# Kernel tuning notes

Hardware: AMD Instinct MI355X
Metric: run time of the kernel (lower is better)

The kernel has to match this reference:

```python
import jax, jax.numpy as jnp
import numpy as np
import math

B, S, D, H = 8, 1024, 1024, 16
HD = D // H  # head_features = 64
SCALE = math.sqrt(HD)


def setup_inputs() -> dict:
    key = jax.random.key(0)
    k0, k1, k2, k3, k4 = jax.random.split(key, 5)
    x = jax.random.normal(k0, (B, S, D), dtype=jnp.float32)
    attn_mask = (jax.random.uniform(k1, (B, S, S)) < 0.9).astype(jnp.float32)
    w_scale = 1.0 / math.sqrt(D)  # keep unsafe exp in finite range
    Wq = jax.random.normal(k2, (D, D), dtype=jnp.float32) * w_scale
    Wk = jax.random.normal(k3, (D, D), dtype=jnp.float32) * w_scale
    Wv = jax.random.normal(k4, (D, D), dtype=jnp.float32) * w_scale
    return {"x": x, "attn_mask": attn_mask, "Wq": Wq, "Wk": Wk, "Wv": Wv}


def reference(x, attn_mask, Wq, Wk, Wv):
    b, s, _ = x.shape

    def split_heads(t):  # [b,s,D] -> [b,H,s,HD]
        return t.reshape(b, s, H, HD).transpose(0, 2, 1, 3)

    q = split_heads(x @ Wq)
    k = split_heads(x @ Wk)
    v = split_heads(x @ Wv)

    # unsafe softmax: exp without max subtraction, multiplicative mask, +1e-8 denom
    scores = jnp.einsum('bhsd,bhtd->bhst', q, k) / SCALE
    e = jnp.exp(scores) * attn_mask[:, None, :, :]
    w = e / (e.sum(axis=3, keepdims=True) + 1e-8)

    ctx = jnp.einsum('bhst,bhtd->bhsd', w, v)  # [b,H,s,HD]
    return ctx.transpose(0, 2, 1, 3).reshape(b, s, D)
```

## Files before the change

### kernel.cpp

```cpp
#include <hip/hip_runtime.h>

#define KDIM 1024

typedef _Float16 half8 __attribute__((ext_vector_type(8)));
typedef _Float16 half4 __attribute__((ext_vector_type(4)));
typedef __fp16 fp16x2 __attribute__((ext_vector_type(2)));
typedef __fp16 fp16x4 __attribute__((ext_vector_type(4)));
typedef float f32x4 __attribute__((ext_vector_type(4)));

#if defined(__has_builtin)
#if __has_builtin(__builtin_amdgcn_global_load_lds)
#define HAVE_GLDS 1
#endif
#if __has_builtin(__builtin_amdgcn_exp2f)
#define EXP2(x) __builtin_amdgcn_exp2f(x)
#endif
#if __has_builtin(__builtin_amdgcn_cvt_pkrtz)
#define HAVE_PKRTZ 1
#endif
#if __has_builtin(__builtin_amdgcn_fdot2)
#define HAVE_FDOT2 1
#endif
#endif
#ifndef EXP2
#define EXP2(x) exp2f(x)
#endif

__device__ __forceinline__ void stage16(const _Float16* g, _Float16* wave_base, int lane) {
#ifdef HAVE_GLDS
  __builtin_amdgcn_global_load_lds(
      (const __attribute__((address_space(1))) void*)g,
      (__attribute__((address_space(3))) void*)wave_base, 16, 0, 0);
#else
  *(half8*)(wave_base + lane * 8) = *(const half8*)g;
#endif
}

__global__ void cast_x_kernel(const float* __restrict__ x, _Float16* __restrict__ xb) {
  size_t i = ((size_t)blockIdx.x * 256 + threadIdx.x) * 4;
  float4 v = *(const float4*)(x + i);
  half4 h = { (_Float16)v.x, (_Float16)v.y, (_Float16)v.z, (_Float16)v.w };
  *(half4*)(xb + i) = h;
}

__global__ void wtrans_kernel(const float* __restrict__ Wq, const float* __restrict__ Wk,
                              const float* __restrict__ Wv, _Float16* __restrict__ Wqkvt) {
  int z = blockIdx.z;
  const float* src = z == 0 ? Wq : (z == 1 ? Wk : Wv);
  _Float16* dst = Wqkvt + (size_t)z * KDIM * KDIM;
  float sc = (z == 0) ? 0.18033688011112042f : 1.0f;
  __shared__ _Float16 tile[32][33];
  int tx = threadIdx.x & 31, ty = threadIdx.x >> 5;
  int c0 = blockIdx.x * 32, r0 = blockIdx.y * 32;
#pragma unroll
  for (int i = 0; i < 4; i++) {
    int r = r0 + ty + i * 8;
    tile[tx][ty + i * 8] = (_Float16)(src[(size_t)r * KDIM + c0 + tx] * sc);
  }
  __syncthreads();
#pragma unroll
  for (int i = 0; i < 4; i++) {
    int n = c0 + ty + i * 8;
    dst[(size_t)n * KDIM + r0 + tx] = tile[ty + i * 8][tx];
  }
}

__global__ void maskbits_kernel(const float* __restrict__ m, unsigned long long* __restrict__ bits) {
  size_t i = (size_t)blockIdx.x * 256 + threadIdx.x;
  unsigned long long b = __ballot(m[i] != 0.0f);
  if ((threadIdx.x & 63) == 0) bits[i >> 6] = b;
}

__global__ __launch_bounds__(256, 2)
void gemm_kernel(const _Float16* __restrict__ A, const _Float16* __restrict__ Bt,
                 _Float16* __restrict__ Qt, _Float16* __restrict__ Kh,
                 _Float16* __restrict__ Vth) {
  __shared__ _Float16 As[128 * 32];
  __shared__ _Float16 Bs[128 * 32];
  int tid = threadIdx.x;
  int lane = tid & 63, w4 = tid >> 6;
  int la = lane & 15, qd = lane >> 4;
  int wm = w4 & 1, wn = w4 >> 1;
  int m0 = blockIdx.y * 128, n0 = blockIdx.x * 128;
  int r = tid >> 2, c = (tid & 3) * 8;
  const _Float16* Ag = A + (size_t)(m0 + r) * KDIM + c;
  const _Float16* Bg = Bt + (size_t)(n0 + r) * KDIM + c;
  _Float16* a0 = As + w4 * 512;
  _Float16* b0 = Bs + w4 * 512;
  f32x4 acc[4][4] = {};
  for (int kt = 0; kt < KDIM; kt += 32) {
    stage16(Ag + kt, a0, lane);
    stage16(Ag + (size_t)64 * KDIM + kt, a0 + 2048, lane);
    stage16(Bg + kt, b0, lane);
    stage16(Bg + (size_t)64 * KDIM + kt, b0 + 2048, lane);
    __syncthreads();
    half8 af[4], bf[4];
#pragma unroll
    for (int mi = 0; mi < 4; mi++)
      af[mi] = *(const half8*)(As + (wm * 64 + mi * 16 + la) * 32 + qd * 8);
#pragma unroll
    for (int ni = 0; ni < 4; ni++)
      bf[ni] = *(const half8*)(Bs + (wn * 64 + ni * 16 + la) * 32 + qd * 8);
#pragma unroll
    for (int mi = 0; mi < 4; mi++)
#pragma unroll
      for (int ni = 0; ni < 4; ni++)
        acc[mi][ni] = __builtin_amdgcn_mfma_f32_16x16x32_f16(af[mi], bf[ni], acc[mi][ni], 0, 0, 0);
    __syncthreads();
  }
  int which = n0 >> 10;
  int hh = ((n0 + wn * 64) >> 6) & 15;
  int mbase = m0 + wm * 64;
  int b = mbase >> 10, s0 = mbase & 1023;
  if (which == 1) {
#pragma unroll
    for (int mi = 0; mi < 4; mi++)
#pragma unroll
      for (int ni = 0; ni < 4; ni++) {
        f32x4 v = acc[mi][ni];
        int s = s0 + mi * 16 + qd * 4;
        int d = ni * 16 + la;
#pragma unroll
        for (int rg = 0; rg < 4; rg++)
          Kh[(((size_t)(b * 16 + hh)) * 1024 + s + rg) * 64 + d] = (_Float16)v[rg];
      }
  } else {
    _Float16* dst = (which == 0) ? Qt : Vth;
    _Float16* ep = (w4 < 2) ? (As + w4 * 2048) : (Bs + (w4 - 2) * 2048);
    _Float16* base = dst + ((size_t)(b * 16 + hh)) * 64 * 1024;
    int rr = lane >> 2, c4 = lane & 3;
#pragma unroll
    for (int ni = 0; ni < 4; ni++) {
#pragma unroll
      for (int mi = 0; mi < 4; mi++) {
        f32x4 v = acc[mi][ni];
        half4 hv = { (_Float16)v[0], (_Float16)v[1], (_Float16)v[2], (_Float16)v[3] };
        *(half4*)(ep + la * 72 + mi * 16 + qd * 4) = hv;
      }
      half8 o0 = *(const half8*)(ep + rr * 72 + c4 * 16);
      half8 o1 = *(const half8*)(ep + rr * 72 + c4 * 16 + 8);
      _Float16* gp = base + (size_t)(ni * 16 + rr) * 1024 + s0 + c4 * 16;
      *(half8*)gp = o0;
      *(half8*)(gp + 8) = o1;
    }
  }
}

__global__ __launch_bounds__(512, 2)
void attn_kernel(const _Float16* __restrict__ Qt, const _Float16* __restrict__ K,
                 const _Float16* __restrict__ Vt, const unsigned long long* __restrict__ mbits,
                 float* __restrict__ out) {
  __shared__ _Float16 Ks[2 * 64 * 32];
  __shared__ _Float16 Vs[2 * 64 * 40];
  int tid = threadIdx.x;
  int lane = tid & 63, w4 = tid >> 6;
  int la = lane & 15, qd = lane >> 4;
  int linear = blockIdx.x;
  int xlo = linear & 7;
  int tmp = linear >> 3;
  int qt = tmp & 7;
  int hb = (tmp >> 3) * 8 + xlo;
  int h = hb & 15, b = hb >> 4;
  const _Float16* Qp = Qt + ((size_t)(b * 16 + h)) * 64 * 1024;
  const _Float16* Kp = K + ((size_t)(b * 16 + h)) * 1024 * 64;
  const _Float16* Vp = Vt + ((size_t)(b * 16 + h)) * 64 * 1024;
  int q0w = qt * 128 + w4 * 16;
  half8 qf[2];
#pragma unroll
  for (int ks = 0; ks < 2; ks++)
#pragma unroll
    for (int j = 0; j < 8; j++)
      qf[ks][j] = Qp[(size_t)(ks * 32 + qd * 8 + j) * 1024 + q0w + la];
  unsigned long long mq[4];
  {
    const ulonglong2* mp =
        (const ulonglong2*)(mbits + ((size_t)b * 1024 + q0w + la) * 16 + qd * 4);
    ulonglong2 m01 = mp[0];
    ulonglong2 m23 = mp[1];
    mq[0] = m01.x; mq[1] = m01.y; mq[2] = m23.x; mq[3] = m23.y;
  }
  f32x4 acco[4] = {};
  float rs = 0.0f;
  int kt_t = (tid & 255) >> 2;
  int kt_d = (tid >> 8) * 32 + (tid & 3) * 8;
  _Float16* kbase = Ks + w4 * 512;
  int vd = tid >> 3;
  int vt = (tid & 7) * 8;
  _Float16* vdst = Vs + (vt >= 32 ? 2560 : 0) + vd * 40 + (vt & 31);
#ifdef HAVE_FDOT2
  fp16x2 one2 = { (__fp16)1.0f, (__fp16)1.0f };
#endif
  for (int tt = 0; tt < 16; tt++) {
    half8 vv = *(const half8*)(Vp + (size_t)vd * 1024 + tt * 64 + vt);
    stage16(Kp + (size_t)(tt * 64 + kt_t) * 64 + kt_d, kbase, lane);
    *(half8*)vdst = vv;
    __syncthreads();
    f32x4 accs[4] = {};
#pragma unroll
    for (int tsub = 0; tsub < 4; tsub++)
#pragma unroll
      for (int ks = 0; ks < 2; ks++) {
        half8 kf = *(const half8*)(Ks + ks * 2048 + (tsub * 16 + la) * 32 + qd * 8);
        accs[tsub] = __builtin_amdgcn_mfma_f32_16x16x32_f16(kf, qf[ks], accs[tsub], 0, 0, 0);
      }
    unsigned long long mw = __shfl(mq[tt & 3], ((tt >> 2) << 4) + la);
#pragma unroll
    for (int tsub = 0; tsub < 4; tsub++) {
      float e0 = ((mw >> (tsub * 16 + qd * 4 + 0)) & 1ull) ? EXP2(accs[tsub][0]) : 0.0f;
      float e1 = ((mw >> (tsub * 16 + qd * 4 + 1)) & 1ull) ? EXP2(accs[tsub][1]) : 0.0f;
      float e2 = ((mw >> (tsub * 16 + qd * 4 + 2)) & 1ull) ? EXP2(accs[tsub][2]) : 0.0f;
      float e3 = ((mw >> (tsub * 16 + qd * 4 + 3)) & 1ull) ? EXP2(accs[tsub][3]) : 0.0f;
      half4 pf;
#ifdef HAVE_PKRTZ
      fp16x2 p01 = __builtin_amdgcn_cvt_pkrtz(e0, e1);
      fp16x2 p23 = __builtin_amdgcn_cvt_pkrtz(e2, e3);
      fp16x4 pfv = __builtin_shufflevector(p01, p23, 0, 1, 2, 3);
      pf = __builtin_bit_cast(half4, pfv);
#else
      pf[0] = (_Float16)e0; pf[1] = (_Float16)e1; pf[2] = (_Float16)e2; pf[3] = (_Float16)e3;
#endif
#if defined(HAVE_FDOT2) && defined(HAVE_PKRTZ)
      rs = __builtin_amdgcn_fdot2(p01, one2, rs, false);
      rs = __builtin_amdgcn_fdot2(p23, one2, rs, false);
#else
      rs += e0 + e1 + e2 + e3;
#endif
#pragma unroll
      for (int nsub = 0; nsub < 4; nsub++) {
        half4 vf = *(const half4*)(Vs + (tsub >> 1) * 2560 + (nsub * 16 + la) * 40 +
                                   (tsub & 1) * 16 + qd * 4);
        acco[nsub] = __builtin_amdgcn_mfma_f32_16x16x16f16(pf, vf, acco[nsub], 0, 0, 0);
      }
    }
    __syncthreads();
  }
  rs += __shfl_xor(rs, 16);
  rs += __shfl_xor(rs, 32);
  float inv_q = 1.0f / (rs + 1e-8f);
  float* op = out + (size_t)b * 1024 * 1024 + (size_t)h * 64;
#pragma unroll
  for (int rg = 0; rg < 4; rg++) {
    float inv = __shfl(inv_q, qd * 4 + rg);
    int s = q0w + qd * 4 + rg;
#pragma unroll
    for (int nsub = 0; nsub < 4; nsub++)
      op[(size_t)s * 1024 + nsub * 16 + la] = acco[nsub][rg] * inv;
  }
}

extern "C" void kernel_launch(void* const* d_in, const int* in_sizes, int n_in,
                              void* d_out, int out_size, void* d_ws, size_t ws_size,
                              hipStream_t stream) {
  (void)in_sizes; (void)n_in; (void)out_size; (void)ws_size;
  const float* x = (const float*)d_in[0];
  const float* am = (const float*)d_in[1];
  const float* Wq = (const float*)d_in[2];
  const float* Wk = (const float*)d_in[3];
  const float* Wv = (const float*)d_in[4];
  float* out = (float*)d_out;

  char* p = (char*)d_ws;
  _Float16* xb = (_Float16*)p;    p += (size_t)8192 * 1024 * 2;
  _Float16* Wqkvt = (_Float16*)p; p += (size_t)3 * 1024 * 1024 * 2;
  _Float16* Qt = (_Float16*)p;    p += (size_t)8192 * 1024 * 2;
  _Float16* Kh = (_Float16*)p;    p += (size_t)8192 * 1024 * 2;
  _Float16* Vth = (_Float16*)p;   p += (size_t)8192 * 1024 * 2;
  unsigned long long* mb = (unsigned long long*)p;

  cast_x_kernel<<<8192, 256, 0, stream>>>(x, xb);
  wtrans_kernel<<<dim3(32, 32, 3), 256, 0, stream>>>(Wq, Wk, Wv, Wqkvt);
  maskbits_kernel<<<32768, 256, 0, stream>>>(am, mb);
  gemm_kernel<<<dim3(24, 64), 256, 0, stream>>>(xb, Wqkvt, Qt, Kh, Vth);
  attn_kernel<<<1024, 512, 0, stream>>>(Qt, Kh, Vth, mb, out);
}
```

Measured before the change: 266.2 us.

## Process two query tiles per wave to reuse staged K/V tiles

Each attention block now covers 256 query rows instead of 128, with every wave holding two 16-row query fragments. Each K/V tile loaded into shared memory serves twice as many queries, and each K fragment read from LDS feeds two MFMAs. This halves the K/V global traffic and staging per query. In exchange the grid shrinks to 512 blocks, which may reduce occupancy and load balance, and register pressure rises under launch_bounds(512,2).

```diff
diff --git a/kernel.cpp b/kernel.cpp
--- a/kernel.cpp
+++ b/kernel.cpp
@@ -158,36 +158,39 @@
   int linear = blockIdx.x;
   int xlo = linear & 7;
   int tmp = linear >> 3;
-  int qt = tmp & 7;
-  int hb = (tmp >> 3) * 8 + xlo;
+  int qt = tmp & 3;
+  int hb = (tmp >> 2) * 8 + xlo;
   int h = hb & 15, b = hb >> 4;
-  const _Float16* Qp = Qt + ((size_t)(b * 16 + h)) * 64 * 1024;
-  const _Float16* Kp = K + ((size_t)(b * 16 + h)) * 1024 * 64;
-  const _Float16* Vp = Vt + ((size_t)(b * 16 + h)) * 64 * 1024;
-  int q0w = qt * 128 + w4 * 16;
-  half8 qf[2];
-#pragma unroll
-  for (int ks = 0; ks < 2; ks++)
-#pragma unroll
-    for (int j = 0; j < 8; j++)
-      qf[ks][j] = Qp[(size_t)(ks * 32 + qd * 8 + j) * 1024 + q0w + la];
-  unsigned long long mq[4];
-  {
+  const _Float16* Qp = Qt + (size_t)hb * 64 * 1024;
+  const _Float16* Kp = K + (size_t)hb * 1024 * 64;
+  const _Float16* Vp = Vt + (size_t)hb * 64 * 1024;
+  int q0w = qt * 256 + w4 * 16;
+  half8 qf[2][2];
+#pragma unroll
+  for (int qi = 0; qi < 2; qi++)
+#pragma unroll
+    for (int ks = 0; ks < 2; ks++)
+#pragma unroll
+      for (int j = 0; j < 8; j++)
+        qf[qi][ks][j] = Qp[(size_t)(ks * 32 + qd * 8 + j) * 1024 + q0w + qi * 128 + la];
+  unsigned long long mq[2][4];
+#pragma unroll
+  for (int qi = 0; qi < 2; qi++) {
     const ulonglong2* mp =
-        (const ulonglong2*)(mbits + ((size_t)b * 1024 + q0w + la) * 16 + qd * 4);
+        (const ulonglong2*)(mbits + ((size_t)b * 1024 + q0w + qi * 128 + la) * 16 + qd * 4);
     ulonglong2 m01 = mp[0];
     ulonglong2 m23 = mp[1];
-    mq[0] = m01.x; mq[1] = m01.y; mq[2] = m23.x; mq[3] = m23.y;
-  }
-  f32x4 acco[4] = {};
-  float rs = 0.0f;
+    mq[qi][0] = m01.x; mq[qi][1] = m01.y; mq[qi][2] = m23.x; mq[qi][3] = m23.y;
+  }
+  f32x4 acco[2][4] = {};
+  float rs[2] = {0.f, 0.f};
   int kt_t = (tid & 255) >> 2;
   int kt_d = (tid >> 8) * 32 + (tid & 3) * 8;
   _Float16* kbase = Ks + w4 * 512;
   int vd = tid >> 3;
   int vt = (tid & 7) * 8;
   _Float16* vdst = Vs + (vt >= 32 ? 2560 : 0) + vd * 40 + (vt & 31);
-#ifdef HAVE_FDOT2
+#if defined(HAVE_FDOT2) && defined(HAVE_PKRTZ)
   fp16x2 one2 = { (__fp16)1.0f, (__fp16)1.0f };
 #endif
   for (int tt = 0; tt < 16; tt++) {
@@ -195,56 +198,67 @@
     stage16(Kp + (size_t)(tt * 64 + kt_t) * 64 + kt_d, kbase, lane);
     *(half8*)vdst = vv;
     __syncthreads();
-    f32x4 accs[4] = {};
-#pragma unroll
-    for (int tsub = 0; tsub < 4; tsub++)
-#pragma unroll
-      for (int ks = 0; ks < 2; ks++) {
-        half8 kf = *(const half8*)(Ks + ks * 2048 + (tsub * 16 + la) * 32 + qd * 8);
-        accs[tsub] = __builtin_amdgcn_mfma_f32_16x16x32_f16(kf, qf[ks], accs[tsub], 0, 0, 0);
-      }
-    unsigned long long mw = __shfl(mq[tt & 3], ((tt >> 2) << 4) + la);
+    unsigned long long mw0 = __shfl(mq[0][tt & 3], ((tt >> 2) << 4) + la);
+    unsigned long long mw1 = __shfl(mq[1][tt & 3], ((tt >> 2) << 4) + la);
 #pragma unroll
     for (int tsub = 0; tsub < 4; tsub++) {
-      float e0 = ((mw >> (tsub * 16 + qd * 4 + 0)) & 1ull) ? EXP2(accs[tsub][0]) : 0.0f;
-      float e1 = ((mw >> (tsub * 16 + qd * 4 + 1)) & 1ull) ? EXP2(accs[tsub][1]) : 0.0f;
-      float e2 = ((mw >> (tsub * 16 + qd * 4 + 2)) & 1ull) ? EXP2(accs[tsub][2]) : 0.0f;
-      float e3 = ((mw >> (tsub * 16 + qd * 4 + 3)) & 1ull) ? EXP2(accs[tsub][3]) : 0.0f;
-      half4 pf;
+      half8 kf0 = *(const half8*)(Ks + (tsub * 16 + la) * 32 + qd * 8);
+      half8 kf1 = *(const half8*)(Ks + 2048 + (tsub * 16 + la) * 32 + qd * 8);
+      f32x4 a0 = {}, a1 = {};
+      a0 = __builtin_amdgcn_mfma_f32_16x16x32_f16(kf0, qf[0][0], a0, 0, 0, 0);
+      a1 = __builtin_amdgcn_mfma_f32_16x16x32_f16(kf0, qf[1][0], a1, 0, 0, 0);
+      a0 = __builtin_amdgcn_mfma_f32_16x16x32_f16(kf1, qf[0][1], a0, 0, 0, 0);
+      a1 = __builtin_amdgcn_mfma_f32_16x16x32_f16(kf1, qf[1][1], a1, 0, 0, 0);
+      half4 pf[2];
+#pragma unroll
+      for (int qi = 0; qi < 2; qi++) {
+        const f32x4& aa = qi ? a1 : a0;
+        unsigned long long mw = qi ? mw1 : mw0;
+        float e0 = ((mw >> (tsub * 16 + qd * 4 + 0)) & 1ull) ? EXP2(aa[0]) : 0.0f;
+        float e1 = ((mw >> (tsub * 16 + qd * 4 + 1)) & 1ull) ? EXP2(aa[1]) : 0.0f;
+        float e2 = ((mw >> (tsub * 16 + qd * 4 + 2)) & 1ull) ? EXP2(aa[2]) : 0.0f;
+        float e3 = ((mw >> (tsub * 16 + qd * 4 + 3)) & 1ull) ? EXP2(aa[3]) : 0.0f;
 #ifdef HAVE_PKRTZ
-      fp16x2 p01 = __builtin_amdgcn_cvt_pkrtz(e0, e1);
-      fp16x2 p23 = __builtin_amdgcn_cvt_pkrtz(e2, e3);
-      fp16x4 pfv = __builtin_shufflevector(p01, p23, 0, 1, 2, 3);
-      pf = __builtin_bit_cast(half4, pfv);
+        fp16x2 p01 = __builtin_amdgcn_cvt_pkrtz(e0, e1);
+        fp16x2 p23 = __builtin_amdgcn_cvt_pkrtz(e2, e3);
+        fp16x4 pfv = __builtin_shufflevector(p01, p23, 0, 1, 2, 3);
+        pf[qi] = __builtin_bit_cast(half4, pfv);
 #else
-      pf[0] = (_Float16)e0; pf[1] = (_Float16)e1; pf[2] = (_Float16)e2; pf[3] = (_Float16)e3;
+        pf[qi][0] = (_Float16)e0; pf[qi][1] = (_Float16)e1;
+        pf[qi][2] = (_Float16)e2; pf[qi][3] = (_Float16)e3;
 #endif
 #if defined(HAVE_FDOT2) && defined(HAVE_PKRTZ)
-      rs = __builtin_amdgcn_fdot2(p01, one2, rs, false);
-      rs = __builtin_amdgcn_fdot2(p23, one2, rs, false);
+        rs[qi] = __builtin_amdgcn_fdot2(p01, one2, rs[qi], false);
+        rs[qi] = __builtin_amdgcn_fdot2(p23, one2, rs[qi], false);
 #else
-      rs += e0 + e1 + e2 + e3;
-#endif
+        rs[qi] += e0 + e1 + e2 + e3;
+#endif
+      }
 #pragma unroll
       for (int nsub = 0; nsub < 4; nsub++) {
         half4 vf = *(const half4*)(Vs + (tsub >> 1) * 2560 + (nsub * 16 + la) * 40 +
                                    (tsub & 1) * 16 + qd * 4);
-        acco[nsub] = __builtin_amdgcn_mfma_f32_16x16x16f16(pf, vf, acco[nsub], 0, 0, 0);
+        acco[0][nsub] = __builtin_amdgcn_mfma_f32_16x16x16f16(pf[0], vf, acco[0][nsub], 0, 0, 0);
+        acco[1][nsub] = __builtin_amdgcn_mfma_f32_16x16x16f16(pf[1], vf, acco[1][nsub], 0, 0, 0);
       }
     }
     __syncthreads();
   }
-  rs += __shfl_xor(rs, 16);
-  rs += __shfl_xor(rs, 32);
-  float inv_q = 1.0f / (rs + 1e-8f);
   float* op = out + (size_t)b * 1024 * 1024 + (size_t)h * 64;
 #pragma unroll
-  for (int rg = 0; rg < 4; rg++) {
-    float inv = __shfl(inv_q, qd * 4 + rg);
-    int s = q0w + qd * 4 + rg;
-#pragma unroll
-    for (int nsub = 0; nsub < 4; nsub++)
-      op[(size_t)s * 1024 + nsub * 16 + la] = acco[nsub][rg] * inv;
+  for (int qi = 0; qi < 2; qi++) {
+    float r0 = rs[qi];
+    r0 += __shfl_xor(r0, 16);
+    r0 += __shfl_xor(r0, 32);
+    float inv_q = 1.0f / (r0 + 1e-8f);
+#pragma unroll
+    for (int rg = 0; rg < 4; rg++) {
+      float inv = __shfl(inv_q, qd * 4 + rg);
+      int s = q0w + qi * 128 + qd * 4 + rg;
+#pragma unroll
+      for (int nsub = 0; nsub < 4; nsub++)
+        op[(size_t)s * 1024 + nsub * 16 + la] = acco[qi][nsub][rg] * inv;
+    }
   }
 }
 
@@ -271,5 +285,5 @@
   wtrans_kernel<<<dim3(32, 32, 3), 256, 0, stream>>>(Wq, Wk, Wv, Wqkvt);
   maskbits_kernel<<<32768, 256, 0, stream>>>(am, mb);
   gemm_kernel<<<dim3(24, 64), 256, 0, stream>>>(xb, Wqkvt, Qt, Kh, Vth);
-  attn_kernel<<<1024, 512, 0, stream>>>(Qt, Kh, Vth, mb, out);
-}
+  attn_kernel<<<512, 512, 0, stream>>>(Qt, Kh, Vth, mb, out);
+}
```

New measurement: 263.4 us. Within noise of the previous version (-1.1%).
